# Kernel tuning notes

Measured on AMD Instinct MI355X. Metric: run time of the kernel, lower is better.

Reference implementation:

```python
import jax, jax.numpy as jnp
import numpy as np

N, E, F, H, L, G = 100000, 1600000, 128, 128, 8, 256
EPS = 1e-5


def setup_inputs() -> dict:
    key = jax.random.key(0)
    ks = jax.random.split(key, 12)
    s = 0.05
    return {
        "x": jax.random.normal(ks[0], (N, F), jnp.float32),
        "edge_index": jax.random.randint(ks[1], (2, E), 0, N, dtype=jnp.int32),
        "batch": jnp.sort(jax.random.randint(ks[2], (N,), 0, G, dtype=jnp.int32)),
        # input projection
        "Wp": jax.random.normal(ks[3], (F, H), jnp.float32) * s,
        "bp": jnp.zeros((H,), jnp.float32),
        # stacked residual-block params (L blocks, 2 GCNConv+BN each)
        "W1": jax.random.normal(ks[4], (L, H, H), jnp.float32) * s,
        "b1": jnp.zeros((L, H), jnp.float32),
        "g1": jnp.ones((L, H), jnp.float32),
        "be1": jnp.zeros((L, H), jnp.float32),
        "W2": jax.random.normal(ks[5], (L, H, H), jnp.float32) * s,
        "b2": jnp.zeros((L, H), jnp.float32),
        "g2": jnp.ones((L, H), jnp.float32),
        "be2": jnp.zeros((L, H), jnp.float32),
        # readout MLP: 3H -> 2H -> H -> 1
        "Wa": jax.random.normal(ks[6], (3 * H, 2 * H), jnp.float32) * s,
        "ba": jnp.zeros((2 * H,), jnp.float32),
        "Wb": jax.random.normal(ks[7], (2 * H, H), jnp.float32) * s,
        "bb": jnp.zeros((H,), jnp.float32),
        "Wc": jax.random.normal(ks[8], (H, 1), jnp.float32) * s,
        "bc": jnp.zeros((1,), jnp.float32),
    }


def _bn(h, g, b):
    # BatchNorm over the node dimension (training-style batch stats, eps=1e-5)
    mu = h.mean(0)
    var = h.var(0)
    return (h - mu) * jax.lax.rsqrt(var + EPS) * g + b


def reference(x, edge_index, batch, Wp, bp, W1, b1, g1, be1, W2, b2, g2, be2,
              Wa, ba, Wb, bb, Wc, bc):
    src, dst = edge_index[0], edge_index[1]
    # GCN symmetric norm with self-loops: deg = in-degree + 1
    deg = jnp.zeros((N,), x.dtype).at[dst].add(1.0) + 1.0
    dinv = jax.lax.rsqrt(deg)
    norm_e = (dinv[src] * dinv[dst])[:, None]   # [E,1]
    self_norm = (dinv * dinv)[:, None]          # [N,1]

    def gcn(h, W, b):
        hw = h @ W                                              # [N,H]
        agg = jnp.zeros_like(hw).at[dst].add(norm_e * hw[src])  # scatter-add over edges
        return agg + self_norm * hw + b                         # self-loop + bias

    h = x @ Wp + bp

    def step(h, p):
        w1, bb1, gg1, bbe1, w2, bb2, gg2, bbe2 = p
        o = jax.nn.relu(_bn(gcn(h, w1, bb1), gg1, bbe1))
        o = _bn(gcn(o, w2, bb2), gg2, bbe2)
        return h + o, None

    h, _ = jax.lax.scan(step, h, (W1, b1, g1, be1, W2, b2, g2, be2))

    sums = jax.ops.segment_sum(h, batch, num_segments=G)
    cnt = jax.ops.segment_sum(jnp.ones((N, 1), h.dtype), batch, num_segments=G)
    mean = sums / jnp.maximum(cnt, 1.0)
    mx = jax.ops.segment_max(h, batch, num_segments=G)
    z = jnp.concatenate([mean, mx, sums], axis=1)  # [G, 3H]

    z = jax.nn.relu(z @ Wa + ba)
    z = jax.nn.relu(z @ Wb + bb)
    return z @ Wc + bc  # [G, 1]
```

## Files before the change

kernel.cpp:

```cpp
#include <hip/hip_runtime.h>
#include <hip/hip_fp16.h>
#include <math.h>
#include <float.h>

#define HDIM 128
#define NGRAPH 256
#define EPSBN 1e-5f
#define PS_REP 32

typedef _Float16 f16x8 __attribute__((ext_vector_type(8)));
typedef _Float16 f16x4 __attribute__((ext_vector_type(4)));
typedef float f32x4 __attribute__((ext_vector_type(4)));

__device__ inline unsigned enc_f(float v) {
  unsigned u = __float_as_uint(v);
  return (u & 0x80000000u) ? ~u : (u | 0x80000000u);
}
__device__ inline float dec_f(unsigned e) {
  return __uint_as_float((e & 0x80000000u) ? (e ^ 0x80000000u) : ~e);
}

__global__ void k_deg(const int* __restrict__ dst, int* __restrict__ deg, int E) {
  int i = blockIdx.x * blockDim.x + threadIdx.x;
  if (i < E) atomicAdd(&deg[dst[i]], 1);
}

__global__ void k_dinv(const int* __restrict__ deg, float* __restrict__ dinv, int n) {
  int i = blockIdx.x * blockDim.x + threadIdx.x;
  if (i < n) dinv[i] = rsqrtf((float)deg[i] + 1.0f);
}

__global__ void k_scanA(const int* __restrict__ deg, int* __restrict__ rowstart,
                        int* __restrict__ bsum, int n) {
  __shared__ int s[256];
  int t = threadIdx.x, i = blockIdx.x * 256 + t;
  int v = (i < n) ? ((deg[i] + 7) & ~7) : 0;
  s[t] = v;
  __syncthreads();
  for (int off = 1; off < 256; off <<= 1) {
    int x = (t >= off) ? s[t - off] : 0;
    __syncthreads();
    s[t] += x;
    __syncthreads();
  }
  if (i < n) rowstart[i] = s[t] - v;
  if (t == 255) bsum[blockIdx.x] = s[255];
}

__global__ void k_scanB(int* __restrict__ bsum, int nb) {
  __shared__ int s[512];
  int t = threadIdx.x;
  int v = (t < nb) ? bsum[t] : 0;
  s[t] = v;
  __syncthreads();
  for (int off = 1; off < 512; off <<= 1) {
    int x = (t >= off) ? s[t - off] : 0;
    __syncthreads();
    s[t] += x;
    __syncthreads();
  }
  if (t < nb) bsum[t] = s[t] - v;
}

__global__ void k_scanC(int* __restrict__ rowstart, const int* __restrict__ bsum,
                        const int* __restrict__ deg, int n) {
  int i = blockIdx.x * 256 + threadIdx.x;
  if (i < n) {
    int v = rowstart[i] + bsum[blockIdx.x];
    rowstart[i] = v;
    if (i == n - 1) rowstart[n] = v + ((deg[i] + 7) & ~7);
  }
}

__global__ void k_fill(const int* __restrict__ src, const int* __restrict__ dst,
                       const float* __restrict__ dinv, const int* __restrict__ prow,
                       int* __restrict__ cursor, int2* __restrict__ csr_sw, int E) {
  int e = blockIdx.x * blockDim.x + threadIdx.x;
  if (e < E) {
    int d = dst[e], s = src[e];
    int pos = prow[d] + atomicAdd(&cursor[d], 1);
    csr_sw[pos] = make_int2(s, __float_as_int(dinv[s] * dinv[d]));
  }
}

__global__ void k_pad(const int* __restrict__ deg, const int* __restrict__ prow,
                      int2* __restrict__ csr_sw, int n) {
  int i = blockIdx.x * blockDim.x + threadIdx.x;
  if (i < n) {
    int d = deg[i], dp = (d + 7) & ~7;
    int base = prow[i];
    for (int j = d; j < dp; ++j) csr_sw[base + j] = make_int2(i, 0);
  }
}

__global__ __launch_bounds__(256) void k_wprep(const float* __restrict__ W1,
                                               const float* __restrict__ W2,
                                               _Float16* __restrict__ wt) {
  int m = blockIdx.x;
  const float* Wsrc = ((m & 1) ? W2 : W1) + (size_t)(m >> 1) * 16384;
  _Float16* Wdst = wt + (size_t)m * 16384;
  __shared__ _Float16 lds[128 * 132];
  int t = threadIdx.x;
  const float4* W4 = (const float4*)Wsrc;
  for (int it = 0; it < 16; ++it) {
    int idx = t + it * 256;
    int k = idx >> 5, c4 = idx & 31;
    float4 v = W4[idx];
    lds[(c4 * 4 + 0) * 132 + k] = (_Float16)v.x;
    lds[(c4 * 4 + 1) * 132 + k] = (_Float16)v.y;
    lds[(c4 * 4 + 2) * 132 + k] = (_Float16)v.z;
    lds[(c4 * 4 + 3) * 132 + k] = (_Float16)v.w;
  }
  __syncthreads();
  for (int it = 0; it < 16; ++it) {
    int idx = t + it * 256;
    int col = idx >> 5, k4 = idx & 31;
    f16x4 o;
    o[0] = lds[col * 132 + k4 * 4 + 0];
    o[1] = lds[col * 132 + k4 * 4 + 1];
    o[2] = lds[col * 132 + k4 * 4 + 2];
    o[3] = lds[col * 132 + k4 * 4 + 3];
    *(f16x4*)(Wdst + col * 128 + k4 * 4) = o;
  }
}

__global__ __launch_bounds__(256) void k_gemmf(const float* __restrict__ in,
                                               const float* __restrict__ W,
                                               const float* __restrict__ bias,
                                               float* __restrict__ out, int n) {
  __shared__ float Ws[64 * 128];
  __shared__ float hs[64 * 68];
  int tid = threadIdx.x;
  int tx = tid & 15;
  int ty = tid >> 4;
  int row0 = blockIdx.x * 64;
  float acc[4][8];
#pragma unroll
  for (int i = 0; i < 4; i++)
#pragma unroll
    for (int j = 0; j < 8; j++) acc[i][j] = 0.f;

  for (int k0 = 0; k0 < 128; k0 += 64) {
    __syncthreads();
    for (int idx = tid; idx < 64 * 128 / 4; idx += 256) {
      float4 v = ((const float4*)(W + k0 * 128))[idx];
      ((float4*)Ws)[idx] = v;
    }
    for (int idx = tid; idx < 64 * 64 / 4; idx += 256) {
      int r = idx >> 4;
      int c4 = idx & 15;
      int row = row0 + r;
      if (row >= n) row = n - 1;
      float4 v = *(const float4*)(in + (size_t)row * 128 + k0 + c4 * 4);
      *(float4*)(hs + r * 68 + c4 * 4) = v;
    }
    __syncthreads();
#pragma unroll
    for (int kk = 0; kk < 64; kk += 4) {
      float4 a[4];
#pragma unroll
      for (int i = 0; i < 4; i++) a[i] = *(const float4*)(hs + (ty + 16 * i) * 68 + kk);
#pragma unroll
      for (int kq = 0; kq < 4; kq++) {
        float4 b0 = *(const float4*)(Ws + (kk + kq) * 128 + tx * 4);
        float4 b1 = *(const float4*)(Ws + (kk + kq) * 128 + 64 + tx * 4);
#pragma unroll
        for (int i = 0; i < 4; i++) {
          float aa = ((const float*)&a[i])[kq];
          acc[i][0] += aa * b0.x; acc[i][1] += aa * b0.y;
          acc[i][2] += aa * b0.z; acc[i][3] += aa * b0.w;
          acc[i][4] += aa * b1.x; acc[i][5] += aa * b1.y;
          acc[i][6] += aa * b1.z; acc[i][7] += aa * b1.w;
        }
      }
    }
  }
#pragma unroll
  for (int i = 0; i < 4; i++) {
    int row = row0 + ty + 16 * i;
    if (row < n) {
      float4 bb0 = *(const float4*)(bias + tx * 4);
      float4 bb1 = *(const float4*)(bias + 64 + tx * 4);
      *(float4*)(out + (size_t)row * 128 + tx * 4) =
          make_float4(acc[i][0] + bb0.x, acc[i][1] + bb0.y, acc[i][2] + bb0.z, acc[i][3] + bb0.w);
      *(float4*)(out + (size_t)row * 128 + 64 + tx * 4) =
          make_float4(acc[i][4] + bb1.x, acc[i][5] + bb1.y, acc[i][6] + bb1.z, acc[i][7] + bb1.w);
    }
  }
}

template <int XFORM>
__global__ __launch_bounds__(256) void k_gemmh(const float* __restrict__ in,
                                               const _Float16* __restrict__ wt,
                                               const float* __restrict__ scale,
                                               const float* __restrict__ shift,
                                               float* __restrict__ hres,
                                               _Float16* __restrict__ outh, int n) {
  __shared__ _Float16 As[64 * 128];
  __shared__ _Float16 Bs[128 * 128];
  char* Ap = (char*)As;
  char* Bp = (char*)Bs;
  int tid = threadIdx.x;
  int lane = tid & 63;
  int rt = tid >> 6;
  int row0 = blockIdx.x * 64;

  for (int it = 0; it < 8; ++it) {
    int idx = tid + it * 256;
    int r = idx >> 5, c4 = idx & 31;
    int rrow = row0 + r;
    int row = (rrow >= n) ? (n - 1) : rrow;
    float4 v = *(const float4*)(in + (size_t)row * 128 + c4 * 4);
    if (XFORM == 1) {
      float4 sc = *(const float4*)(scale + c4 * 4);
      float4 sh = *(const float4*)(shift + c4 * 4);
      v.x = fmaxf(v.x * sc.x + sh.x, 0.f);
      v.y = fmaxf(v.y * sc.y + sh.y, 0.f);
      v.z = fmaxf(v.z * sc.z + sh.z, 0.f);
      v.w = fmaxf(v.w * sc.w + sh.w, 0.f);
    }
    if (XFORM == 2) {
      float4 sc = *(const float4*)(scale + c4 * 4);
      float4 sh = *(const float4*)(shift + c4 * 4);
      float4 hv = *(const float4*)(hres + (size_t)row * 128 + c4 * 4);
      v.x = v.x * sc.x + sh.x + hv.x;
      v.y = v.y * sc.y + sh.y + hv.y;
      v.z = v.z * sc.z + sh.z + hv.z;
      v.w = v.w * sc.w + sh.w + hv.w;
      if (rrow < n) *(float4*)(hres + (size_t)row * 128 + c4 * 4) = v;
    }
    f16x4 hv16;
    hv16[0] = (_Float16)v.x; hv16[1] = (_Float16)v.y;
    hv16[2] = (_Float16)v.z; hv16[3] = (_Float16)v.w;
    *(f16x4*)(Ap + ((r * 256 + c4 * 8) ^ ((r & 7) << 4))) = hv16;
  }
  for (int it = 0; it < 8; ++it) {
    int idx = tid + it * 256;
    int col = idx >> 4, k8 = idx & 15;
    f16x8 v = *(const f16x8*)(wt + col * 128 + k8 * 8);
    *(f16x8*)(Bp + ((col * 256 + k8 * 16) ^ ((col & 7) << 4))) = v;
  }
  __syncthreads();

  f32x4 acc[8];
#pragma unroll
  for (int ct = 0; ct < 8; ++ct) acc[ct] = (f32x4){0.f, 0.f, 0.f, 0.f};

  int arow = rt * 16 + (lane & 15);
  int kc = (lane >> 4) * 16;
#pragma unroll
  for (int ks = 0; ks < 4; ++ks) {
    int kb = ks * 64;
    f16x8 a = *(f16x8*)(Ap + ((arow * 256 + kb + kc) ^ ((arow & 7) << 4)));
#pragma unroll
    for (int ct = 0; ct < 8; ++ct) {
      int bcol = ct * 16 + (lane & 15);
      f16x8 b = *(f16x8*)(Bp + ((bcol * 256 + kb + kc) ^ ((bcol & 7) << 4)));
      acc[ct] = __builtin_amdgcn_mfma_f32_16x16x32_f16(a, b, acc[ct], 0, 0, 0);
    }
  }

  int orow0 = row0 + rt * 16 + (lane >> 4) * 4;
#pragma unroll
  for (int ct = 0; ct < 8; ++ct) {
    int col = ct * 16 + (lane & 15);
#pragma unroll
    for (int r = 0; r < 4; ++r) {
      int row = orow0 + r;
      if (row < n) outh[(size_t)row * 128 + col] = (_Float16)acc[ct][r];
    }
  }
}

__global__ __launch_bounds__(256) void k_agg(const _Float16* __restrict__ hw,
                                             const int* __restrict__ prow,
                                             const int4* __restrict__ csr4,
                                             const float* __restrict__ dinv,
                                             const float* __restrict__ bias,
                                             float* __restrict__ out,
                                             float* __restrict__ psum,
                                             float* __restrict__ psq, int n) {
  int wave = threadIdx.x >> 6;
  int lane = threadIdx.x & 63;
  int half = lane >> 5;
  int l32 = lane & 31;
  int node = blockIdx.x * 4 + wave;
  float r0 = 0.f, r1 = 0.f, r2 = 0.f, r3 = 0.f;
  if (node < n) {
    int q0 = prow[node] >> 1, q1 = prow[node + 1] >> 1;
    float a0[4] = {0, 0, 0, 0}, a1[4] = {0, 0, 0, 0};
    float a2[4] = {0, 0, 0, 0}, a3[4] = {0, 0, 0, 0};
    for (int q = q0; q < q1; q += 4) {
      int4 p0 = csr4[q], p1 = csr4[q + 1], p2 = csr4[q + 2], p3 = csr4[q + 3];
      int s0 = half ? p0.z : p0.x;  float w0 = __int_as_float(half ? p0.w : p0.y);
      int s1 = half ? p1.z : p1.x;  float w1 = __int_as_float(half ? p1.w : p1.y);
      int s2 = half ? p2.z : p2.x;  float w2 = __int_as_float(half ? p2.w : p2.y);
      int s3 = half ? p3.z : p3.x;  float w3 = __int_as_float(half ? p3.w : p3.y);
      f16x4 v0 = *(const f16x4*)(hw + (size_t)s0 * 128 + l32 * 4);
      f16x4 v1 = *(const f16x4*)(hw + (size_t)s1 * 128 + l32 * 4);
      f16x4 v2 = *(const f16x4*)(hw + (size_t)s2 * 128 + l32 * 4);
      f16x4 v3 = *(const f16x4*)(hw + (size_t)s3 * 128 + l32 * 4);
#pragma unroll
      for (int j = 0; j < 4; ++j) {
        a0[j] += w0 * (float)v0[j];
        a1[j] += w1 * (float)v1[j];
        a2[j] += w2 * (float)v2[j];
        a3[j] += w3 * (float)v3[j];
      }
    }
    r0 = (a0[0] + a1[0]) + (a2[0] + a3[0]);
    r1 = (a0[1] + a1[1]) + (a2[1] + a3[1]);
    r2 = (a0[2] + a1[2]) + (a2[2] + a3[2]);
    r3 = (a0[3] + a1[3]) + (a2[3] + a3[3]);
    r0 += __shfl_xor(r0, 32);
    r1 += __shfl_xor(r1, 32);
    r2 += __shfl_xor(r2, 32);
    r3 += __shfl_xor(r3, 32);
    float dn = dinv[node];
    float sn = dn * dn;
    f16x4 v = *(const f16x4*)(hw + (size_t)node * 128 + l32 * 4);
    float4 bb = *(const float4*)(bias + l32 * 4);
    r0 += sn * (float)v[0] + bb.x;
    r1 += sn * (float)v[1] + bb.y;
    r2 += sn * (float)v[2] + bb.z;
    r3 += sn * (float)v[3] + bb.w;
    if (half == 0)
      *(float4*)(out + (size_t)node * 128 + l32 * 4) = make_float4(r0, r1, r2, r3);
  }
  __shared__ float ss[4][128];
  __shared__ float sq[4][128];
  if (half == 0) {
    float vv0 = (node < n) ? r0 : 0.f;
    float vv1 = (node < n) ? r1 : 0.f;
    float vv2 = (node < n) ? r2 : 0.f;
    float vv3 = (node < n) ? r3 : 0.f;
    *(float4*)&ss[wave][l32 * 4] = make_float4(vv0, vv1, vv2, vv3);
    *(float4*)&sq[wave][l32 * 4] = make_float4(vv0 * vv0, vv1 * vv1, vv2 * vv2, vv3 * vv3);
  }
  __syncthreads();
  int t = threadIdx.x;
  if (t < 128) {
    float s = (ss[0][t] + ss[1][t]) + (ss[2][t] + ss[3][t]);
    float q = (sq[0][t] + sq[1][t]) + (sq[2][t] + sq[3][t]);
    int rep = blockIdx.x & (PS_REP - 1);
    atomicAdd(&psum[rep * 128 + t], s);
    atomicAdd(&psq[rep * 128 + t], q);
  }
}

__global__ void k_bnfin(float* __restrict__ psum, float* __restrict__ psq,
                        const float* __restrict__ g, const float* __restrict__ be,
                        float* __restrict__ scale, float* __restrict__ shift, int n) {
  int c = threadIdx.x;
  float s = 0.f, q = 0.f;
  for (int r = 0; r < PS_REP; ++r) {
    s += psum[r * 128 + c];
    q += psq[r * 128 + c];
    psum[r * 128 + c] = 0.f;
    psq[r * 128 + c] = 0.f;
  }
  float mu = s / (float)n;
  float var = q / (float)n - mu * mu;
  float rs = rsqrtf(var + EPSBN);
  float sc = g[c] * rs;
  scale[c] = sc;
  shift[c] = be[c] - mu * sc;
}

__global__ __launch_bounds__(256) void k_bnresid(const float* __restrict__ x,
                                                 const float* __restrict__ scale,
                                                 const float* __restrict__ shift,
                                                 float* __restrict__ out, int n) {
  int idx = blockIdx.x * 256 + threadIdx.x;
  int total = n * 32;
  if (idx >= total) return;
  int c4 = idx & 31;
  float4 v = ((const float4*)x)[idx];
  float4 sc = ((const float4*)scale)[c4];
  float4 sh = ((const float4*)shift)[c4];
  float4 h = ((const float4*)out)[idx];
  ((float4*)out)[idx] = make_float4(v.x * sc.x + sh.x + h.x, v.y * sc.y + sh.y + h.y,
                                    v.z * sc.z + sh.z + h.z, v.w * sc.w + sh.w + h.w);
}

#define PCHUNK 128
__global__ __launch_bounds__(128) void k_pool(const float* __restrict__ h,
                                              const int* __restrict__ batch,
                                              float* __restrict__ sums,
                                              unsigned* __restrict__ maxenc,
                                              int* __restrict__ cnt, int n) {
  int c = threadIdx.x;
  int start = blockIdx.x * PCHUNK;
  if (start >= n) return;
  int end = start + PCHUNK;
  if (end > n) end = n;
  int cur = batch[start];
  float s = 0.f, mx = -FLT_MAX;
  int runlen = 0;
  for (int i = start; i < end; ++i) {
    int b = batch[i];
    if (b != cur) {
      atomicAdd(&sums[cur * 128 + c], s);
      atomicMax(&maxenc[cur * 128 + c], enc_f(mx));
      if (c == 0) atomicAdd(&cnt[cur], runlen);
      s = 0.f; mx = -FLT_MAX; runlen = 0; cur = b;
    }
    float v = h[(size_t)i * 128 + c];
    s += v;
    mx = fmaxf(mx, v);
    runlen++;
  }
  atomicAdd(&sums[cur * 128 + c], s);
  atomicMax(&maxenc[cur * 128 + c], enc_f(mx));
  if (c == 0) atomicAdd(&cnt[cur], runlen);
}

__global__ __launch_bounds__(256) void k_readout(const float* __restrict__ sums,
                                                 const unsigned* __restrict__ maxenc,
                                                 const int* __restrict__ cnt,
                                                 const float* __restrict__ Wa,
                                                 const float* __restrict__ ba,
                                                 const float* __restrict__ Wb,
                                                 const float* __restrict__ bb,
                                                 const float* __restrict__ Wc,
                                                 const float* __restrict__ bc,
                                                 float* __restrict__ out) {
  int g = blockIdx.x;
  int t = threadIdx.x;
  __shared__ float z[384];
  __shared__ float za[256];
  __shared__ float zb[128];
  float c = (float)(cnt[g] > 1 ? cnt[g] : 1);
  if (t < 128) {
    float s = sums[g * 128 + t];
    z[t] = s / c;
    z[128 + t] = dec_f(maxenc[g * 128 + t]);
    z[256 + t] = s;
  }
  __syncthreads();
  float accA = ba[t];
  for (int k = 0; k < 384; k++) accA += z[k] * Wa[k * 256 + t];
  za[t] = fmaxf(accA, 0.f);
  __syncthreads();
  if (t < 128) {
    float accB = bb[t];
    for (int k = 0; k < 256; k++) accB += za[k] * Wb[k * 128 + t];
    zb[t] = fmaxf(accB, 0.f);
  }
  __syncthreads();
  if (t < 64) {
    float p = zb[t] * Wc[t] + zb[t + 64] * Wc[t + 64];
    for (int off = 32; off > 0; off >>= 1) p += __shfl_down(p, off);
    if (t == 0) out[g] = p + bc[0];
  }
}

extern "C" void kernel_launch(void* const* d_in, const int* in_sizes, int n_in,
                              void* d_out, int out_size, void* d_ws, size_t ws_size,
                              hipStream_t stream) {
  const float* x   = (const float*)d_in[0];
  const int* edge  = (const int*)d_in[1];
  const int* batch = (const int*)d_in[2];
  const float* Wp  = (const float*)d_in[3];
  const float* bp  = (const float*)d_in[4];
  const float* W1  = (const float*)d_in[5];
  const float* b1  = (const float*)d_in[6];
  const float* g1  = (const float*)d_in[7];
  const float* be1 = (const float*)d_in[8];
  const float* W2  = (const float*)d_in[9];
  const float* b2  = (const float*)d_in[10];
  const float* g2  = (const float*)d_in[11];
  const float* be2 = (const float*)d_in[12];
  const float* Wa  = (const float*)d_in[13];
  const float* ba  = (const float*)d_in[14];
  const float* Wb  = (const float*)d_in[15];
  const float* bbp = (const float*)d_in[16];
  const float* Wc  = (const float*)d_in[17];
  const float* bc  = (const float*)d_in[18];
  float* out = (float*)d_out;

  const int N = in_sizes[0] / 128;
  const int E = in_sizes[1] / 2;
  const int* esrc = edge;
  const int* edst = edge + E;

  char* p = (char*)d_ws;
  auto carve = [&](size_t bytes) {
    char* r = p;
    p += (bytes + 255) & ~(size_t)255;
    return (void*)r;
  };
  float* h    = (float*)carve((size_t)N * 128 * 4);
  _Float16* t1h = (_Float16*)carve((size_t)N * 128 * 2);
  float* t2   = (float*)carve((size_t)N * 128 * 4);
  int2* csr_sw = (int2*)carve(((size_t)E + 8 * (size_t)N) * 8);
  int* deg     = (int*)carve((size_t)N * 4);
  float* dinv  = (float*)carve((size_t)N * 4);
  int* prow    = (int*)carve((size_t)(N + 1) * 4);
  int* cursor  = (int*)carve((size_t)N * 4);
  int* bsum    = (int*)carve(512 * 4);
  float* psum  = (float*)carve((size_t)PS_REP * 128 * 2 * 4);
  float* psq   = psum + PS_REP * 128;
  float* scale = (float*)carve(128 * 4);
  float* shift = (float*)carve(128 * 4);
  float* pools = (float*)carve((size_t)NGRAPH * 128 * 4);
  unsigned* poolm = (unsigned*)carve((size_t)NGRAPH * 128 * 4);
  int* poolc      = (int*)carve(NGRAPH * 4);
  _Float16* wt16  = (_Float16*)carve((size_t)16 * 128 * 128 * 2);

  const int NB = (N + 255) / 256;

  hipMemsetAsync(deg, 0, (size_t)N * 4, stream);
  hipMemsetAsync(cursor, 0, (size_t)N * 4, stream);
  hipMemsetAsync(psum, 0, (size_t)PS_REP * 128 * 2 * 4, stream);
  hipMemsetAsync(pools, 0, (size_t)NGRAPH * 128 * 4, stream);
  hipMemsetAsync(poolm, 0, (size_t)NGRAPH * 128 * 4, stream);
  hipMemsetAsync(poolc, 0, (size_t)NGRAPH * 4, stream);

  k_deg<<<(E + 255) / 256, 256, 0, stream>>>(edst, deg, E);
  k_dinv<<<NB, 256, 0, stream>>>(deg, dinv, N);
  k_scanA<<<NB, 256, 0, stream>>>(deg, prow, bsum, N);
  k_scanB<<<1, 512, 0, stream>>>(bsum, NB);
  k_scanC<<<NB, 256, 0, stream>>>(prow, bsum, deg, N);
  k_fill<<<(E + 255) / 256, 256, 0, stream>>>(esrc, edst, dinv, prow, cursor, csr_sw, E);
  k_pad<<<NB, 256, 0, stream>>>(deg, prow, csr_sw, N);
  k_wprep<<<16, 256, 0, stream>>>(W1, W2, wt16);

  const int GB = (N + 63) / 64;
  const int AB = (N + 3) / 4;
  const int EB = (N * 32 + 255) / 256;
  const int PB = (N + PCHUNK - 1) / PCHUNK;

  k_gemmf<<<GB, 256, 0, stream>>>(x, Wp, bp, h, N);

  for (int l = 0; l < 8; l++) {
    const _Float16* w1t = wt16 + (size_t)(l * 2) * 16384;
    const _Float16* w2t = wt16 + (size_t)(l * 2 + 1) * 16384;
    if (l == 0) {
      k_gemmh<0><<<GB, 256, 0, stream>>>(h, w1t, nullptr, nullptr, nullptr, t1h, N);
    }
    k_agg<<<AB, 256, 0, stream>>>(t1h, prow, (const int4*)csr_sw, dinv, b1 + l * 128, t2, psum, psq, N);
    k_bnfin<<<1, 128, 0, stream>>>(psum, psq, g1 + l * 128, be1 + l * 128, scale, shift, N);
    k_gemmh<1><<<GB, 256, 0, stream>>>(t2, w2t, scale, shift, nullptr, t1h, N);
    k_agg<<<AB, 256, 0, stream>>>(t1h, prow, (const int4*)csr_sw, dinv, b2 + l * 128, t2, psum, psq, N);
    k_bnfin<<<1, 128, 0, stream>>>(psum, psq, g2 + l * 128, be2 + l * 128, scale, shift, N);
    if (l < 7) {
      const _Float16* w1n = wt16 + (size_t)((l + 1) * 2) * 16384;
      k_gemmh<2><<<GB, 256, 0, stream>>>(t2, w1n, scale, shift, h, t1h, N);
    } else {
      k_bnresid<<<EB, 256, 0, stream>>>(t2, scale, shift, h, N);
    }
  }

  k_pool<<<PB, 128, 0, stream>>>(h, batch, pools, poolm, poolc, N);
  k_readout<<<NGRAPH, 256, 0, stream>>>(pools, poolm, poolc, Wa, ba, Wb, bbp, Wc, bc, out);
}
```

Baseline: 1.935 ms.

## Fuse BN finalize into consumers, MFMA input projection, wider gather in aggregation

Removes the separate single-block BN-finalize kernels by recomputing scale/shift in each consumer (gemmh and pool) from per-layer partial-sum slabs, which also drops the in-kernel zeroing. The final BN+residual kernel is folded into the pooling kernel. The fp32 input projection GEMM is replaced by an fp16 MFMA kernel using a pre-converted Wp. The aggregation kernel now has four 16-lane groups each gathering 8 halfs per edge, for more edges in flight. Costs are redundant per-block stats reduction and extra fp16 rounding in the projection.

Result: faster. 1.873 ms (-3.2%).

```diff
diff --git a/kernel.cpp b/kernel.cpp
--- a/kernel.cpp
+++ b/kernel.cpp
@@ -7,6 +7,7 @@
 #define NGRAPH 256
 #define EPSBN 1e-5f
 #define PS_REP 32
+#define SLABF (2 * PS_REP * 128)
 
 typedef _Float16 f16x8 __attribute__((ext_vector_type(8)));
 typedef _Float16 f16x4 __attribute__((ext_vector_type(4)));
@@ -95,9 +96,10 @@
 
 __global__ __launch_bounds__(256) void k_wprep(const float* __restrict__ W1,
                                                const float* __restrict__ W2,
+                                               const float* __restrict__ Wp,
                                                _Float16* __restrict__ wt) {
   int m = blockIdx.x;
-  const float* Wsrc = ((m & 1) ? W2 : W1) + (size_t)(m >> 1) * 16384;
+  const float* Wsrc = (m == 16) ? Wp : (((m & 1) ? W2 : W1) + (size_t)(m >> 1) * 16384);
   _Float16* Wdst = wt + (size_t)m * 16384;
   __shared__ _Float16 lds[128 * 132];
   int t = threadIdx.x;
@@ -124,78 +126,10 @@
   }
 }
 
-__global__ __launch_bounds__(256) void k_gemmf(const float* __restrict__ in,
-                                               const float* __restrict__ W,
+__global__ __launch_bounds__(256) void k_gemmp(const float* __restrict__ in,
+                                               const _Float16* __restrict__ wt,
                                                const float* __restrict__ bias,
                                                float* __restrict__ out, int n) {
-  __shared__ float Ws[64 * 128];
-  __shared__ float hs[64 * 68];
-  int tid = threadIdx.x;
-  int tx = tid & 15;
-  int ty = tid >> 4;
-  int row0 = blockIdx.x * 64;
-  float acc[4][8];
-#pragma unroll
-  for (int i = 0; i < 4; i++)
-#pragma unroll
-    for (int j = 0; j < 8; j++) acc[i][j] = 0.f;
-
-  for (int k0 = 0; k0 < 128; k0 += 64) {
-    __syncthreads();
-    for (int idx = tid; idx < 64 * 128 / 4; idx += 256) {
-      float4 v = ((const float4*)(W + k0 * 128))[idx];
-      ((float4*)Ws)[idx] = v;
-    }
-    for (int idx = tid; idx < 64 * 64 / 4; idx += 256) {
-      int r = idx >> 4;
-      int c4 = idx & 15;
-      int row = row0 + r;
-      if (row >= n) row = n - 1;
-      float4 v = *(const float4*)(in + (size_t)row * 128 + k0 + c4 * 4);
-      *(float4*)(hs + r * 68 + c4 * 4) = v;
-    }
-    __syncthreads();
-#pragma unroll
-    for (int kk = 0; kk < 64; kk += 4) {
-      float4 a[4];
-#pragma unroll
-      for (int i = 0; i < 4; i++) a[i] = *(const float4*)(hs + (ty + 16 * i) * 68 + kk);
-#pragma unroll
-      for (int kq = 0; kq < 4; kq++) {
-        float4 b0 = *(const float4*)(Ws + (kk + kq) * 128 + tx * 4);
-        float4 b1 = *(const float4*)(Ws + (kk + kq) * 128 + 64 + tx * 4);
-#pragma unroll
-        for (int i = 0; i < 4; i++) {
-          float aa = ((const float*)&a[i])[kq];
-          acc[i][0] += aa * b0.x; acc[i][1] += aa * b0.y;
-          acc[i][2] += aa * b0.z; acc[i][3] += aa * b0.w;
-          acc[i][4] += aa * b1.x; acc[i][5] += aa * b1.y;
-          acc[i][6] += aa * b1.z; acc[i][7] += aa * b1.w;
-        }
-      }
-    }
-  }
-#pragma unroll
-  for (int i = 0; i < 4; i++) {
-    int row = row0 + ty + 16 * i;
-    if (row < n) {
-      float4 bb0 = *(const float4*)(bias + tx * 4);
-      float4 bb1 = *(const float4*)(bias + 64 + tx * 4);
-      *(float4*)(out + (size_t)row * 128 + tx * 4) =
-          make_float4(acc[i][0] + bb0.x, acc[i][1] + bb0.y, acc[i][2] + bb0.z, acc[i][3] + bb0.w);
-      *(float4*)(out + (size_t)row * 128 + 64 + tx * 4) =
-          make_float4(acc[i][4] + bb1.x, acc[i][5] + bb1.y, acc[i][6] + bb1.z, acc[i][7] + bb1.w);
-    }
-  }
-}
-
-template <int XFORM>
-__global__ __launch_bounds__(256) void k_gemmh(const float* __restrict__ in,
-                                               const _Float16* __restrict__ wt,
-                                               const float* __restrict__ scale,
-                                               const float* __restrict__ shift,
-                                               float* __restrict__ hres,
-                                               _Float16* __restrict__ outh, int n) {
   __shared__ _Float16 As[64 * 128];
   __shared__ _Float16 Bs[128 * 128];
   char* Ap = (char*)As;
@@ -208,20 +142,106 @@
   for (int it = 0; it < 8; ++it) {
     int idx = tid + it * 256;
     int r = idx >> 5, c4 = idx & 31;
+    int row = row0 + r;
+    if (row >= n) row = n - 1;
+    float4 v = *(const float4*)(in + (size_t)row * 128 + c4 * 4);
+    f16x4 hv;
+    hv[0] = (_Float16)v.x; hv[1] = (_Float16)v.y;
+    hv[2] = (_Float16)v.z; hv[3] = (_Float16)v.w;
+    *(f16x4*)(Ap + ((r * 256 + c4 * 8) ^ ((r & 7) << 4))) = hv;
+  }
+  for (int it = 0; it < 8; ++it) {
+    int idx = tid + it * 256;
+    int col = idx >> 4, k8 = idx & 15;
+    f16x8 v = *(const f16x8*)(wt + col * 128 + k8 * 8);
+    *(f16x8*)(Bp + ((col * 256 + k8 * 16) ^ ((col & 7) << 4))) = v;
+  }
+  __syncthreads();
+
+  f32x4 acc[8];
+#pragma unroll
+  for (int ct = 0; ct < 8; ++ct) acc[ct] = (f32x4){0.f, 0.f, 0.f, 0.f};
+  int arow = rt * 16 + (lane & 15);
+  int kc = (lane >> 4) * 16;
+#pragma unroll
+  for (int ks = 0; ks < 4; ++ks) {
+    int kb = ks * 64;
+    f16x8 a = *(f16x8*)(Ap + ((arow * 256 + kb + kc) ^ ((arow & 7) << 4)));
+#pragma unroll
+    for (int ct = 0; ct < 8; ++ct) {
+      int bcol = ct * 16 + (lane & 15);
+      f16x8 b = *(f16x8*)(Bp + ((bcol * 256 + kb + kc) ^ ((bcol & 7) << 4)));
+      acc[ct] = __builtin_amdgcn_mfma_f32_16x16x32_f16(a, b, acc[ct], 0, 0, 0);
+    }
+  }
+
+  int orow0 = row0 + rt * 16 + (lane >> 4) * 4;
+#pragma unroll
+  for (int ct = 0; ct < 8; ++ct) {
+    int col = ct * 16 + (lane & 15);
+    float bb = bias[col];
+#pragma unroll
+    for (int r = 0; r < 4; ++r) {
+      int row = orow0 + r;
+      if (row < n) out[(size_t)row * 128 + col] = acc[ct][r] + bb;
+    }
+  }
+}
+
+template <int XFORM>
+__global__ __launch_bounds__(256) void k_gemmh(const float* __restrict__ in,
+                                               const _Float16* __restrict__ wt,
+                                               const float* __restrict__ psumL,
+                                               const float* __restrict__ gg,
+                                               const float* __restrict__ be,
+                                               float* __restrict__ hres,
+                                               _Float16* __restrict__ outh, int n) {
+  __shared__ _Float16 As[64 * 128];
+  __shared__ _Float16 Bs[128 * 128];
+  __shared__ float sc_s[128], sh_s[128];
+  char* Ap = (char*)As;
+  char* Bp = (char*)Bs;
+  int tid = threadIdx.x;
+  int lane = tid & 63;
+  int rt = tid >> 6;
+  int row0 = blockIdx.x * 64;
+
+  if (XFORM) {
+    if (tid < 128) {
+      const float* psqL = psumL + PS_REP * 128;
+      float s = 0.f, q = 0.f;
+#pragma unroll 8
+      for (int r = 0; r < PS_REP; ++r) {
+        s += psumL[r * 128 + tid];
+        q += psqL[r * 128 + tid];
+      }
+      float mu = s / (float)n;
+      float var = q / (float)n - mu * mu;
+      float rs = rsqrtf(var + EPSBN);
+      float sc = gg[tid] * rs;
+      sc_s[tid] = sc;
+      sh_s[tid] = be[tid] - mu * sc;
+    }
+    __syncthreads();
+  }
+
+  for (int it = 0; it < 8; ++it) {
+    int idx = tid + it * 256;
+    int r = idx >> 5, c4 = idx & 31;
     int rrow = row0 + r;
     int row = (rrow >= n) ? (n - 1) : rrow;
     float4 v = *(const float4*)(in + (size_t)row * 128 + c4 * 4);
     if (XFORM == 1) {
-      float4 sc = *(const float4*)(scale + c4 * 4);
-      float4 sh = *(const float4*)(shift + c4 * 4);
+      float4 sc = *(const float4*)(sc_s + c4 * 4);
+      float4 sh = *(const float4*)(sh_s + c4 * 4);
       v.x = fmaxf(v.x * sc.x + sh.x, 0.f);
       v.y = fmaxf(v.y * sc.y + sh.y, 0.f);
       v.z = fmaxf(v.z * sc.z + sh.z, 0.f);
       v.w = fmaxf(v.w * sc.w + sh.w, 0.f);
     }
     if (XFORM == 2) {
-      float4 sc = *(const float4*)(scale + c4 * 4);
-      float4 sh = *(const float4*)(shift + c4 * 4);
+      float4 sc = *(const float4*)(sc_s + c4 * 4);
+      float4 sh = *(const float4*)(sh_s + c4 * 4);
       float4 hv = *(const float4*)(hres + (size_t)row * 128 + c4 * 4);
       v.x = v.x * sc.x + sh.x + hv.x;
       v.y = v.y * sc.y + sh.y + hv.y;
@@ -278,64 +298,72 @@
                                              const float* __restrict__ dinv,
                                              const float* __restrict__ bias,
                                              float* __restrict__ out,
-                                             float* __restrict__ psum,
-                                             float* __restrict__ psq, int n) {
+                                             float* __restrict__ psumL, int n) {
   int wave = threadIdx.x >> 6;
   int lane = threadIdx.x & 63;
-  int half = lane >> 5;
-  int l32 = lane & 31;
+  int grp = lane >> 4;
+  int l16 = lane & 15;
   int node = blockIdx.x * 4 + wave;
-  float r0 = 0.f, r1 = 0.f, r2 = 0.f, r3 = 0.f;
+  float a[8];
+#pragma unroll
+  for (int j = 0; j < 8; ++j) a[j] = 0.f;
+
   if (node < n) {
+    float b8[8];
+#pragma unroll
+    for (int j = 0; j < 8; ++j) b8[j] = 0.f;
     int q0 = prow[node] >> 1, q1 = prow[node + 1] >> 1;
-    float a0[4] = {0, 0, 0, 0}, a1[4] = {0, 0, 0, 0};
-    float a2[4] = {0, 0, 0, 0}, a3[4] = {0, 0, 0, 0};
     for (int q = q0; q < q1; q += 4) {
       int4 p0 = csr4[q], p1 = csr4[q + 1], p2 = csr4[q + 2], p3 = csr4[q + 3];
-      int s0 = half ? p0.z : p0.x;  float w0 = __int_as_float(half ? p0.w : p0.y);
-      int s1 = half ? p1.z : p1.x;  float w1 = __int_as_float(half ? p1.w : p1.y);
-      int s2 = half ? p2.z : p2.x;  float w2 = __int_as_float(half ? p2.w : p2.y);
-      int s3 = half ? p3.z : p3.x;  float w3 = __int_as_float(half ? p3.w : p3.y);
-      f16x4 v0 = *(const f16x4*)(hw + (size_t)s0 * 128 + l32 * 4);
-      f16x4 v1 = *(const f16x4*)(hw + (size_t)s1 * 128 + l32 * 4);
-      f16x4 v2 = *(const f16x4*)(hw + (size_t)s2 * 128 + l32 * 4);
-      f16x4 v3 = *(const f16x4*)(hw + (size_t)s3 * 128 + l32 * 4);
-#pragma unroll
-      for (int j = 0; j < 4; ++j) {
-        a0[j] += w0 * (float)v0[j];
-        a1[j] += w1 * (float)v1[j];
-        a2[j] += w2 * (float)v2[j];
-        a3[j] += w3 * (float)v3[j];
+      int4 pa = (grp & 2) ? p1 : p0;
+      int4 pb = (grp & 2) ? p3 : p2;
+      int sa = (grp & 1) ? pa.z : pa.x;
+      float wa = __int_as_float((grp & 1) ? pa.w : pa.y);
+      int sb = (grp & 1) ? pb.z : pb.x;
+      float wb = __int_as_float((grp & 1) ? pb.w : pb.y);
+      f16x8 va = *(const f16x8*)(hw + (size_t)sa * 128 + l16 * 8);
+      f16x8 vb = *(const f16x8*)(hw + (size_t)sb * 128 + l16 * 8);
+#pragma unroll
+      for (int j = 0; j < 8; ++j) {
+        a[j] += wa * (float)va[j];
+        b8[j] += wb * (float)vb[j];
       }
     }
-    r0 = (a0[0] + a1[0]) + (a2[0] + a3[0]);
-    r1 = (a0[1] + a1[1]) + (a2[1] + a3[1]);
-    r2 = (a0[2] + a1[2]) + (a2[2] + a3[2]);
-    r3 = (a0[3] + a1[3]) + (a2[3] + a3[3]);
-    r0 += __shfl_xor(r0, 32);
-    r1 += __shfl_xor(r1, 32);
-    r2 += __shfl_xor(r2, 32);
-    r3 += __shfl_xor(r3, 32);
+#pragma unroll
+    for (int j = 0; j < 8; ++j) a[j] += b8[j];
+#pragma unroll
+    for (int j = 0; j < 8; ++j) {
+      a[j] += __shfl_xor(a[j], 16);
+      a[j] += __shfl_xor(a[j], 32);
+    }
     float dn = dinv[node];
     float sn = dn * dn;
-    f16x4 v = *(const f16x4*)(hw + (size_t)node * 128 + l32 * 4);
-    float4 bb = *(const float4*)(bias + l32 * 4);
-    r0 += sn * (float)v[0] + bb.x;
-    r1 += sn * (float)v[1] + bb.y;
-    r2 += sn * (float)v[2] + bb.z;
-    r3 += sn * (float)v[3] + bb.w;
-    if (half == 0)
-      *(float4*)(out + (size_t)node * 128 + l32 * 4) = make_float4(r0, r1, r2, r3);
+    f16x8 v = *(const f16x8*)(hw + (size_t)node * 128 + l16 * 8);
+    float4 bb0 = *(const float4*)(bias + l16 * 8);
+    float4 bb1 = *(const float4*)(bias + l16 * 8 + 4);
+    a[0] += sn * (float)v[0] + bb0.x;
+    a[1] += sn * (float)v[1] + bb0.y;
+    a[2] += sn * (float)v[2] + bb0.z;
+    a[3] += sn * (float)v[3] + bb0.w;
+    a[4] += sn * (float)v[4] + bb1.x;
+    a[5] += sn * (float)v[5] + bb1.y;
+    a[6] += sn * (float)v[6] + bb1.z;
+    a[7] += sn * (float)v[7] + bb1.w;
+    if (grp == 0) {
+      *(float4*)(out + (size_t)node * 128 + l16 * 8) = make_float4(a[0], a[1], a[2], a[3]);
+      *(float4*)(out + (size_t)node * 128 + l16 * 8 + 4) = make_float4(a[4], a[5], a[6], a[7]);
+    }
   }
   __shared__ float ss[4][128];
   __shared__ float sq[4][128];
-  if (half == 0) {
-    float vv0 = (node < n) ? r0 : 0.f;
-    float vv1 = (node < n) ? r1 : 0.f;
-    float vv2 = (node < n) ? r2 : 0.f;
-    float vv3 = (node < n) ? r3 : 0.f;
-    *(float4*)&ss[wave][l32 * 4] = make_float4(vv0, vv1, vv2, vv3);
-    *(float4*)&sq[wave][l32 * 4] = make_float4(vv0 * vv0, vv1 * vv1, vv2 * vv2, vv3 * vv3);
+  if (grp == 0) {
+    bool live = (node < n);
+#pragma unroll
+    for (int j = 0; j < 8; ++j) {
+      float v = live ? a[j] : 0.f;
+      ss[wave][l16 * 8 + j] = v;
+      sq[wave][l16 * 8 + j] = v * v;
+    }
   }
   __syncthreads();
   int t = threadIdx.x;
@@ -343,53 +371,41 @@
     float s = (ss[0][t] + ss[1][t]) + (ss[2][t] + ss[3][t]);
     float q = (sq[0][t] + sq[1][t]) + (sq[2][t] + sq[3][t]);
     int rep = blockIdx.x & (PS_REP - 1);
-    atomicAdd(&psum[rep * 128 + t], s);
-    atomicAdd(&psq[rep * 128 + t], q);
-  }
-}
-
-__global__ void k_bnfin(float* __restrict__ psum, float* __restrict__ psq,
-                        const float* __restrict__ g, const float* __restrict__ be,
-                        float* __restrict__ scale, float* __restrict__ shift, int n) {
-  int c = threadIdx.x;
-  float s = 0.f, q = 0.f;
-  for (int r = 0; r < PS_REP; ++r) {
-    s += psum[r * 128 + c];
-    q += psq[r * 128 + c];
-    psum[r * 128 + c] = 0.f;
-    psq[r * 128 + c] = 0.f;
-  }
-  float mu = s / (float)n;
-  float var = q / (float)n - mu * mu;
-  float rs = rsqrtf(var + EPSBN);
-  float sc = g[c] * rs;
-  scale[c] = sc;
-  shift[c] = be[c] - mu * sc;
-}
-
-__global__ __launch_bounds__(256) void k_bnresid(const float* __restrict__ x,
-                                                 const float* __restrict__ scale,
-                                                 const float* __restrict__ shift,
-                                                 float* __restrict__ out, int n) {
-  int idx = blockIdx.x * 256 + threadIdx.x;
-  int total = n * 32;
-  if (idx >= total) return;
-  int c4 = idx & 31;
-  float4 v = ((const float4*)x)[idx];
-  float4 sc = ((const float4*)scale)[c4];
-  float4 sh = ((const float4*)shift)[c4];
-  float4 h = ((const float4*)out)[idx];
-  ((float4*)out)[idx] = make_float4(v.x * sc.x + sh.x + h.x, v.y * sc.y + sh.y + h.y,
-                                    v.z * sc.z + sh.z + h.z, v.w * sc.w + sh.w + h.w);
+    atomicAdd(&psumL[rep * 128 + t], s);
+    atomicAdd(&psumL[PS_REP * 128 + rep * 128 + t], q);
+  }
 }
 
 #define PCHUNK 128
 __global__ __launch_bounds__(128) void k_pool(const float* __restrict__ h,
+                                              const float* __restrict__ t2,
+                                              const float* __restrict__ psumL,
+                                              const float* __restrict__ gg,
+                                              const float* __restrict__ be,
                                               const int* __restrict__ batch,
                                               float* __restrict__ sums,
                                               unsigned* __restrict__ maxenc,
                                               int* __restrict__ cnt, int n) {
   int c = threadIdx.x;
+  __shared__ float sc_s[128], sh_s[128];
+  {
+    const float* psqL = psumL + PS_REP * 128;
+    float s = 0.f, q = 0.f;
+#pragma unroll 8
+    for (int r = 0; r < PS_REP; ++r) {
+      s += psumL[r * 128 + c];
+      q += psqL[r * 128 + c];
+    }
+    float mu = s / (float)n;
+    float var = q / (float)n - mu * mu;
+    float rs = rsqrtf(var + EPSBN);
+    float sc = gg[c] * rs;
+    sc_s[c] = sc;
+    sh_s[c] = be[c] - mu * sc;
+  }
+  __syncthreads();
+  float scc = sc_s[c], shc = sh_s[c];
+
   int start = blockIdx.x * PCHUNK;
   if (start >= n) return;
   int end = start + PCHUNK;
@@ -405,7 +421,7 @@
       if (c == 0) atomicAdd(&cnt[cur], runlen);
       s = 0.f; mx = -FLT_MAX; runlen = 0; cur = b;
     }
-    float v = h[(size_t)i * 128 + c];
+    float v = h[(size_t)i * 128 + c] + scc * t2[(size_t)i * 128 + c] + shc;
     s += v;
     mx = fmaxf(mx, v);
     runlen++;
@@ -499,20 +515,17 @@
   int* prow    = (int*)carve((size_t)(N + 1) * 4);
   int* cursor  = (int*)carve((size_t)N * 4);
   int* bsum    = (int*)carve(512 * 4);
-  float* psum  = (float*)carve((size_t)PS_REP * 128 * 2 * 4);
-  float* psq   = psum + PS_REP * 128;
-  float* scale = (float*)carve(128 * 4);
-  float* shift = (float*)carve(128 * 4);
+  float* slab  = (float*)carve((size_t)16 * SLABF * 4);
   float* pools = (float*)carve((size_t)NGRAPH * 128 * 4);
   unsigned* poolm = (unsigned*)carve((size_t)NGRAPH * 128 * 4);
   int* poolc      = (int*)carve(NGRAPH * 4);
-  _Float16* wt16  = (_Float16*)carve((size_t)16 * 128 * 128 * 2);
+  _Float16* wt16  = (_Float16*)carve((size_t)17 * 128 * 128 * 2);
 
   const int NB = (N + 255) / 256;
 
   hipMemsetAsync(deg, 0, (size_t)N * 4, stream);
   hipMemsetAsync(cursor, 0, (size_t)N * 4, stream);
-  hipMemsetAsync(psum, 0, (size_t)PS_REP * 128 * 2 * 4, stream);
+  hipMemsetAsync(slab, 0, (size_t)16 * SLABF * 4, stream);
   hipMemsetAsync(pools, 0, (size_t)NGRAPH * 128 * 4, stream);
   hipMemsetAsync(poolm, 0, (size_t)NGRAPH * 128 * 4, stream);
   hipMemsetAsync(poolc, 0, (size_t)NGRAPH * 4, stream);
@@ -524,34 +537,29 @@
   k_scanC<<<NB, 256, 0, stream>>>(prow, bsum, deg, N);
   k_fill<<<(E + 255) / 256, 256, 0, stream>>>(esrc, edst, dinv, prow, cursor, csr_sw, E);
   k_pad<<<NB, 256, 0, stream>>>(deg, prow, csr_sw, N);
-  k_wprep<<<16, 256, 0, stream>>>(W1, W2, wt16);
+  k_wprep<<<17, 256, 0, stream>>>(W1, W2, Wp, wt16);
 
   const int GB = (N + 63) / 64;
   const int AB = (N + 3) / 4;
-  const int EB = (N * 32 + 255) / 256;
   const int PB = (N + PCHUNK - 1) / PCHUNK;
 
-  k_gemmf<<<GB, 256, 0, stream>>>(x, Wp, bp, h, N);
+  k_gemmp<<<GB, 256, 0, stream>>>(x, wt16 + (size_t)16 * 16384, bp, h, N);
+  k_gemmh<0><<<GB, 256, 0, stream>>>(h, wt16, nullptr, nullptr, nullptr, nullptr, t1h, N);
 
   for (int l = 0; l < 8; l++) {
-    const _Float16* w1t = wt16 + (size_t)(l * 2) * 16384;
     const _Float16* w2t = wt16 + (size_t)(l * 2 + 1) * 16384;
-    if (l == 0) {
-      k_gemmh<0><<<GB, 256, 0, stream>>>(h, w1t, nullptr, nullptr, nullptr, t1h, N);
-    }
-    k_agg<<<AB, 256, 0, stream>>>(t1h, prow, (const int4*)csr_sw, dinv, b1 + l * 128, t2, psum, psq, N);
-    k_bnfin<<<1, 128, 0, stream>>>(psum, psq, g1 + l * 128, be1 + l * 128, scale, shift, N);
-    k_gemmh<1><<<GB, 256, 0, stream>>>(t2, w2t, scale, shift, nullptr, t1h, N);
-    k_agg<<<AB, 256, 0, stream>>>(t1h, prow, (const int4*)csr_sw, dinv, b2 + l * 128, t2, psum, psq, N);
-    k_bnfin<<<1, 128, 0, stream>>>(psum, psq, g2 + l * 128, be2 + l * 128, scale, shift, N);
+    float* slab1 = slab + (size_t)(2 * l) * SLABF;
+    float* slab2 = slab + (size_t)(2 * l + 1) * SLABF;
+    k_agg<<<AB, 256, 0, stream>>>(t1h, prow, (const int4*)csr_sw, dinv, b1 + l * 128, t2, slab1, N);
+    k_gemmh<1><<<GB, 256, 0, stream>>>(t2, w2t, slab1, g1 + l * 128, be1 + l * 128, nullptr, t1h, N);
+    k_agg<<<AB, 256, 0, stream>>>(t1h, prow, (const int4*)csr_sw, dinv, b2 + l * 128, t2, slab2, N);
     if (l < 7) {
       const _Float16* w1n = wt16 + (size_t)((l + 1) * 2) * 16384;
-      k_gemmh<2><<<GB, 256, 0, stream>>>(t2, w1n, scale, shift, h, t1h, N);
-    } else {
-      k_bnresid<<<EB, 256, 0, stream>>>(t2, scale, shift, h, N);
-    }
-  }
-
-  k_pool<<<PB, 128, 0, stream>>>(h, batch, pools, poolm, poolc, N);
+      k_gemmh<2><<<GB, 256, 0, stream>>>(t2, w1n, slab2, g2 + l * 128, be2 + l * 128, h, t1h, N);
+    }
+  }
+
+  k_pool<<<PB, 128, 0, stream>>>(h, t2, slab + (size_t)15 * SLABF, g2 + 7 * 128, be2 + 7 * 128,
+                                 batch, pools, poolm, poolc, N);
   k_readout<<<NGRAPH, 256, 0, stream>>>(pools, poolm, poolc, Wa, ba, Wb, bbp, Wc, bc, out);
 }
```
